# Kernel tuning notes

Measured on AMD Instinct MI355X. Metric: run time of the kernel, lower is better.

The kernel has to match this reference:

```python
import jax, jax.numpy as jnp
import numpy as np

DEPTH = 17                 # levels of the complete binary tree
N = 2**DEPTH - 1           # 131071 nodes, BFS order: children of n are 2n+1, 2n+2
IN_DIM = 128
HID = 128
OUT = 128


def setup_inputs() -> dict:
    key = jax.random.key(0)
    ks = jax.random.split(key, 20)

    def lin_w(k, o, i):
        s = 1.0 / np.sqrt(i)
        return jax.random.uniform(k, (o, i), minval=-s, maxval=s, dtype=jnp.float32)

    def lin_b(k, o, i):
        s = 1.0 / np.sqrt(i)
        return jax.random.uniform(k, (o,), minval=-s, maxval=s, dtype=jnp.float32)

    inp = {"x": jax.random.normal(ks[0], (N, IN_DIM), dtype=jnp.float32)}
    # complete binary tree, parent -> child edges (row0=src/parent, row1=dst/child)
    child = np.arange(1, N)
    parent = (child - 1) // 2
    inp["edge_index"] = jnp.asarray(np.stack([parent, child]), dtype=jnp.int32)
    names = [("Wi", "bWi", IN_DIM), ("Ui", "bUi", HID),
             ("Wf", "bWf", IN_DIM), ("Uf", "bUf", HID),
             ("Wo", "bWo", IN_DIM), ("Uo", "bUo", HID),
             ("Wu", "bWu", IN_DIM), ("Uu", "bUu", HID)]
    ki = 1
    for wname, bname, idim in names:
        inp[wname] = lin_w(ks[ki], HID, idim)
        inp[bname] = lin_b(ks[ki + 1], HID, idim)
        ki += 2
    inp["Wp"] = lin_w(ks[17], OUT, HID)
    inp["bWp"] = lin_b(ks[18], OUT, HID)
    return inp


def reference(x, edge_index, Wi, bWi, Ui, bUi, Wf, bWf, Uf, bUf,
              Wo, bWo, Uo, bUo, Wu, bWu, Uu, bUu, Wp, bWp):
    # edge_index encodes the complete binary tree in BFS order (children of n
    # are 2n+1 and 2n+2), so the recursion batches exactly by tree level.
    # Precompute input-side gate projections for ALL nodes in 4 GEMMs
    # (equivalent to calling W_*(x[node]) per node in the torch recursion).
    xi = x @ Wi.T + bWi            # (N, H)
    xf = x @ Wf.T + bWf
    xo = x @ Wo.T + bWo
    xu = x @ Wu.T + bWu

    h_next = None  # hidden states of the level below (children)
    c_next = None
    for d in range(DEPTH - 1, -1, -1):   # bottom-up over tree levels
        s = 2**d - 1                     # first node index of level d
        cnt = 2**d                       # nodes at level d
        li, lf, lo, lu = xi[s:s + cnt], xf[s:s + cnt], xo[s:s + cnt], xu[s:s + cnt]
        if h_next is None:               # leaves: no children, h_sum = 0
            i = jax.nn.sigmoid(li)
            o = jax.nn.sigmoid(lo)
            u = jnp.tanh(lu)
            c = i * u
        else:
            # children of node s+k are at positions 2(s+k)+1, 2(s+k)+2: contiguous
            ch_h = h_next.reshape(cnt, 2, HID)
            ch_c = c_next.reshape(cnt, 2, HID)
            h_sum = ch_h.sum(axis=1)     # child-sum
            i = jax.nn.sigmoid(li + h_sum @ Ui.T + bUi)
            o = jax.nn.sigmoid(lo + h_sum @ Uo.T + bUo)
            u = jnp.tanh(lu + h_sum @ Uu.T + bUu)
            # per-child forget gates: sigmoid(W_f x + U_f h_k)
            f = jax.nn.sigmoid(lf[:, None, :] + jnp.einsum('nkh,gh->nkg', ch_h, Uf) + bUf)
            c = i * u + (f * ch_c).sum(axis=1)
        h = o * jnp.tanh(c)
        h_next, c_next = h, c

    h_root = h_next[0]                   # root node index 0
    # dropout is identity in eval mode
    return h_root @ Wp.T + bWp           # (OUT,)
```

## Files before the change

kernel.cpp:

```cpp
#include <hip/hip_runtime.h>
#include <hip/hip_bf16.h>


#define DEPTH 17
#define NTREE ((1 << DEPTH) - 1)
#define DIM 128
#define XSTR 136
#define HSTR 136
#define CSTR 132

typedef __attribute__((ext_vector_type(8))) short short8;
typedef __attribute__((ext_vector_type(4))) float float4v;

__device__ __forceinline__ float sigm(float v) {
    return __fdividef(1.0f, 1.0f + __expf(-v));
}
__device__ __forceinline__ float ftanh(float v) {
    v = fminf(15.0f, fmaxf(-15.0f, v));
    float e = __expf(2.0f * v);
    return __fdividef(e - 1.0f, e + 1.0f);
}

__device__ __forceinline__ unsigned short f2bf(float f) {
    union { float f; unsigned u; } a; a.f = f;
    unsigned u = a.u;
    return (unsigned short)((u + 0x7fffu + ((u >> 16) & 1u)) >> 16);
}
__device__ __forceinline__ float bf2f(unsigned short s) {
    union { unsigned u; float f; } a; a.u = ((unsigned)s) << 16;
    return a.f;
}

struct WPtrs {
    const float* W[4];  const float* U[4];
    const float* bW[4]; const float* bU[4];
};

__global__ __launch_bounds__(256) void prep_kernel(WPtrs p, unsigned short* __restrict__ Bsw,
                                                   float* __restrict__ biasWU, float* __restrict__ biasL) {
    int idx = blockIdx.x * 256 + threadIdx.x;
    int j = idx & 7;
    int lane = (idx >> 3) & 63;
    int g = (idx >> 9) & 3;
    int ks = (idx >> 11) & 7;
    int w = idx >> 14;
    int L = lane & 15, q = lane >> 4;
    int c = w * 16 + L;
    int k = ks * 32 + q * 8 + j;
    float v = (k < 128) ? p.W[g][c * 128 + k] * (g == 3 ? 1.0f : 0.5f)
                        : p.U[g][c * 128 + (k - 128)];
    Bsw[idx] = f2bf(v);
    if (idx < 512) {
        int gg = idx >> 7, cc = idx & 127;
        biasWU[idx] = p.bW[gg][cc] + p.bU[gg][cc];
        biasL[idx]  = p.bW[gg][cc];
    }
}

__global__ __launch_bounds__(256) void convx_kernel(const float* __restrict__ x,
                                                    unsigned short* __restrict__ xbf, int n4) {
    int i = blockIdx.x * 256 + threadIdx.x;
    int stride = gridDim.x * 256;
    for (; i < n4; i += stride) {
        float4 v = ((const float4*)x)[i];
        ushort4 o;
        o.x = f2bf(v.x); o.y = f2bf(v.y); o.z = f2bf(v.z); o.w = f2bf(v.w);
        ((ushort4*)xbf)[i] = o;
    }
}

template <bool LEAF0>
__global__ __launch_bounds__(512, 2) void kd2_kernel(
    const unsigned short* __restrict__ xbf, const unsigned short* __restrict__ Bsw,
    const float* __restrict__ biasL, const float* __restrict__ biasWU,
    unsigned short* __restrict__ hbf, float* __restrict__ cbuf,
    int x0base, int x1base) {
    __shared__ __align__(16) unsigned short xs[48 * XSTR];
    __shared__ __align__(16) unsigned short hc[LEAF0 ? 16 : 64 * XSTR];
    __shared__ __align__(16) unsigned short h0[32 * XSTR];
    __shared__ __align__(16) unsigned short c0[32 * XSTR];
    __shared__ __align__(16) unsigned short hA1[16 * XSTR];
    __shared__ __align__(16) float cA1[16 * CSTR];

    const int tid = threadIdx.x;
    const int w = tid >> 6, lane = tid & 63, L = lane & 15, q = lane >> 4;
    const int ch = w * 16 + L;

    short8 b[32];
#pragma unroll
    for (int t = 0; t < 32; ++t)
        b[t] = *(const short8*)(Bsw + ((size_t)w << 14) + (t << 9) + lane * 8);

    const long n0 = (long)x0base + (long)blockIdx.x * 32;
    const long n1 = (long)x1base + (long)blockIdx.x * 16;
    const long cb = 2 * n0 + 1;

    for (int i = tid; i < 48 * 16; i += 512) {
        const int row = i >> 4, g = i & 15;
        const long node = (row < 32) ? (n0 + row) : (n1 + (row - 32));
        *(uint4*)(xs + row * XSTR + g * 8) = *(const uint4*)(xbf + (size_t)node * DIM + g * 8);
    }
    if (!LEAF0) {
        for (int i = tid; i < 64 * 16; i += 512) {
            const int row = i >> 4, g = i & 15;
            *(uint4*)(hc + row * XSTR + g * 8) = *(const uint4*)(hbf + (size_t)(cb + row) * DIM + g * 8);
        }
    }
    __syncthreads();

    if (LEAF0) {
        float4v acc[2][3];
#pragma unroll
        for (int mm = 0; mm < 2; ++mm)
#pragma unroll
            for (int g = 0; g < 3; ++g) acc[mm][g] = (float4v){0.f, 0.f, 0.f, 0.f};
#pragma unroll
        for (int ks = 0; ks < 4; ++ks) {
            short8 a[2];
            a[0] = *(const short8*)(xs + L * XSTR + ks * 32 + q * 8);
            a[1] = *(const short8*)(xs + (16 + L) * XSTR + ks * 32 + q * 8);
#pragma unroll
            for (int g = 0; g < 3; ++g)
#pragma unroll
                for (int mm = 0; mm < 2; ++mm)
                    acc[mm][g] = __builtin_amdgcn_mfma_f32_16x16x32_bf16(a[mm], b[ks * 4 + g], acc[mm][g], 0, 0, 0);
        }
#pragma unroll
        for (int mm = 0; mm < 2; ++mm)
#pragma unroll
            for (int r = 0; r < 4; ++r) {
                const int nl = 16 * mm + q * 4 + r;
                float iv = sigm(2.f * acc[mm][0][r] + biasL[ch]);
                float ov = sigm(2.f * acc[mm][1][r] + biasL[128 + ch]);
                float uv = ftanh(2.f * acc[mm][2][r] + biasL[256 + ch]);
                float cv = iv * uv;
                c0[nl * XSTR + ch] = f2bf(cv);
                h0[nl * XSTR + ch] = f2bf(ov * ftanh(cv));
            }
    } else {
        for (int mc = 0; mc < 4; mc += 2) {
            float4v acc[2][4];
#pragma unroll
            for (int mm = 0; mm < 2; ++mm)
#pragma unroll
                for (int g = 0; g < 4; ++g) acc[mm][g] = (float4v){0.f, 0.f, 0.f, 0.f};
#pragma unroll
            for (int ks = 0; ks < 8; ++ks) {
                const int kk = ks * 32;
                short8 a[2];
#pragma unroll
                for (int mm = 0; mm < 2; ++mm) {
                    if (kk < 128)
                        a[mm] = *(const short8*)(xs + (8 * (mc + mm) + (L >> 1)) * XSTR + kk + q * 8);
                    else
                        a[mm] = *(const short8*)(hc + (16 * (mc + mm) + L) * XSTR + (kk - 128) + q * 8);
                }
#pragma unroll
                for (int g = 0; g < 4; ++g)
#pragma unroll
                    for (int mm = 0; mm < 2; ++mm)
                        acc[mm][g] = __builtin_amdgcn_mfma_f32_16x16x32_bf16(a[mm], b[ks * 4 + g], acc[mm][g], 0, 0, 0);
            }
#pragma unroll
            for (int mm = 0; mm < 2; ++mm)
#pragma unroll
                for (int e = 0; e < 2; ++e) {
                    const int nl = 8 * (mc + mm) + 2 * q + e;
                    const int r0 = 2 * e, r1 = 2 * e + 1;
                    float iv = sigm(acc[mm][0][r0] + acc[mm][0][r1] + biasWU[ch]);
                    float ov = sigm(acc[mm][1][r0] + acc[mm][1][r1] + biasWU[128 + ch]);
                    float uv = ftanh(acc[mm][2][r0] + acc[mm][2][r1] + biasWU[256 + ch]);
                    float fl = sigm(acc[mm][3][r0] + biasWU[384 + ch]);
                    float fr = sigm(acc[mm][3][r1] + biasWU[384 + ch]);
                    float cl = cbuf[(size_t)(cb + 2 * nl) * DIM + ch];
                    float cr = cbuf[(size_t)(cb + 2 * nl + 1) * DIM + ch];
                    float cv = iv * uv + fl * cl + fr * cr;
                    c0[nl * XSTR + ch] = f2bf(cv);
                    h0[nl * XSTR + ch] = f2bf(ov * ftanh(cv));
                }
        }
    }
    __syncthreads();

    {
        float4v acc[2][4];
#pragma unroll
        for (int mm = 0; mm < 2; ++mm)
#pragma unroll
            for (int g = 0; g < 4; ++g) acc[mm][g] = (float4v){0.f, 0.f, 0.f, 0.f};
#pragma unroll
        for (int ks = 0; ks < 8; ++ks) {
            const int kk = ks * 32;
            short8 a[2];
#pragma unroll
            for (int mm = 0; mm < 2; ++mm) {
                if (kk < 128)
                    a[mm] = *(const short8*)(xs + (32 + 8 * mm + (L >> 1)) * XSTR + kk + q * 8);
                else
                    a[mm] = *(const short8*)(h0 + (16 * mm + L) * XSTR + (kk - 128) + q * 8);
            }
#pragma unroll
            for (int g = 0; g < 4; ++g)
#pragma unroll
                for (int mm = 0; mm < 2; ++mm)
                    acc[mm][g] = __builtin_amdgcn_mfma_f32_16x16x32_bf16(a[mm], b[ks * 4 + g], acc[mm][g], 0, 0, 0);
        }
#pragma unroll
        for (int mm = 0; mm < 2; ++mm)
#pragma unroll
            for (int e = 0; e < 2; ++e) {
                const int nl = 8 * mm + 2 * q + e;
                const int r0 = 2 * e, r1 = 2 * e + 1;
                float iv = sigm(acc[mm][0][r0] + acc[mm][0][r1] + biasWU[ch]);
                float ov = sigm(acc[mm][1][r0] + acc[mm][1][r1] + biasWU[128 + ch]);
                float uv = ftanh(acc[mm][2][r0] + acc[mm][2][r1] + biasWU[256 + ch]);
                float fl = sigm(acc[mm][3][r0] + biasWU[384 + ch]);
                float fr = sigm(acc[mm][3][r1] + biasWU[384 + ch]);
                float cl = bf2f(c0[(2 * nl) * XSTR + ch]);
                float cr = bf2f(c0[(2 * nl + 1) * XSTR + ch]);
                float cv = iv * uv + fl * cl + fr * cr;
                cA1[nl * CSTR + ch] = cv;
                hA1[nl * XSTR + ch] = f2bf(ov * ftanh(cv));
            }
    }
    __syncthreads();

    for (int i = tid; i < 16 * 16; i += 512) {
        const int row = i >> 4, g = i & 15;
        *(uint4*)(hbf + (size_t)(n1 + row) * DIM + g * 8) = *(const uint4*)(hA1 + row * XSTR + g * 8);
    }
    for (int i = tid; i < 16 * 32; i += 512) {
        const int row = i >> 5, j = i & 31;
        *(float4*)(cbuf + (size_t)(n1 + row) * DIM + j * 4) = *(const float4*)(cA1 + row * CSTR + j * 4);
    }
}

template <bool GCH>
__device__ __forceinline__ void internal_level(
    const unsigned short* xc,
    const unsigned short* hin_l, const float* cin_l,
    const unsigned short* __restrict__ hin_g, const float* __restrict__ cin_g, long cb,
    unsigned short* ho, int ho_str, float* co, int co_str, int cnt,
    const short8 (&b)[32], const float* __restrict__ biasWU,
    int L, int q, int ch) {
    const int rows = 2 * cnt;
    const int mt = (rows + 15) >> 4;
    for (int mc = 0; mc < mt; mc += 2) {
        const int mm_n = (mt - mc >= 2) ? 2 : 1;
        float4v acc[2][4];
#pragma unroll
        for (int mm = 0; mm < 2; ++mm)
#pragma unroll
            for (int g = 0; g < 4; ++g) acc[mm][g] = (float4v){0.f, 0.f, 0.f, 0.f};
#pragma unroll
        for (int ks = 0; ks < 8; ++ks) {
            const int kk = ks * 32;
            short8 a[2];
#pragma unroll
            for (int mm = 0; mm < 2; ++mm) {
                if (mm < mm_n) {
                    if (kk < 128) {
                        int xr = 8 * (mc + mm) + (L >> 1);
                        if (xr >= cnt) xr = 0;
                        a[mm] = *(const short8*)(xc + xr * XSTR + kk + q * 8);
                    } else if (!GCH) {
                        a[mm] = *(const short8*)(hin_l + (16 * (mc + mm) + L) * HSTR + (kk - 128) + q * 8);
                    } else {
                        a[mm] = *(const short8*)(hin_g + (size_t)(cb + 16 * (mc + mm) + L) * DIM + (kk - 128) + q * 8);
                    }
                }
            }
#pragma unroll
            for (int g = 0; g < 4; ++g)
#pragma unroll
                for (int mm = 0; mm < 2; ++mm)
                    if (mm < mm_n)
                        acc[mm][g] = __builtin_amdgcn_mfma_f32_16x16x32_bf16(a[mm], b[ks * 4 + g], acc[mm][g], 0, 0, 0);
        }
#pragma unroll
        for (int mm = 0; mm < 2; ++mm)
#pragma unroll
            for (int e = 0; e < 2; ++e) {
                if (mm < mm_n) {
                    const int nl = 8 * (mc + mm) + 2 * q + e;
                    if (nl < cnt) {
                        const int r0 = 2 * e, r1 = 2 * e + 1;
                        float iv = sigm(acc[mm][0][r0] + acc[mm][0][r1] + biasWU[ch]);
                        float ov = sigm(acc[mm][1][r0] + acc[mm][1][r1] + biasWU[128 + ch]);
                        float uv = ftanh(acc[mm][2][r0] + acc[mm][2][r1] + biasWU[256 + ch]);
                        float fl = sigm(acc[mm][3][r0] + biasWU[384 + ch]);
                        float fr = sigm(acc[mm][3][r1] + biasWU[384 + ch]);
                        float cl, cr;
                        if (!GCH) {
                            cl = cin_l[(2 * nl) * CSTR + ch];
                            cr = cin_l[(2 * nl + 1) * CSTR + ch];
                        } else {
                            cl = cin_g[(size_t)(cb + 2 * nl) * DIM + ch];
                            cr = cin_g[(size_t)(cb + 2 * nl + 1) * DIM + ch];
                        }
                        float cv = iv * uv + fl * cl + fr * cr;
                        co[nl * co_str + ch] = cv;
                        ho[nl * ho_str + ch] = f2bf(ov * ftanh(cv));
                    }
                }
            }
    }
}

template <int C, int NL, bool PROJ>
__global__ __launch_bounds__(512, 2) void k23_kernel(
    const unsigned short* __restrict__ xbf, const unsigned short* __restrict__ Bsw,
    const float* __restrict__ biasWU, unsigned short* __restrict__ hbf,
    float* __restrict__ cbuf, int d0,
    const float* __restrict__ Wp, const float* __restrict__ bWp,
    float* __restrict__ out) {
    constexpr int TOTX = 2 * C - (C >> (NL - 1));
    constexpr int AR = (C < 16) ? 16 : C;
    __shared__ __align__(16) unsigned short xs[TOTX * XSTR];
    __shared__ __align__(16) unsigned short hA[AR * HSTR];
    __shared__ __align__(16) unsigned short hB[16 * HSTR];
    __shared__ __align__(16) float cA[AR * CSTR];
    __shared__ __align__(16) float cB[16 * CSTR];
    __shared__ float red[4][128];

    const int tid = threadIdx.x;
    const int w = tid >> 6, lane = tid & 63, L = lane & 15, q = lane >> 4;
    const int ch = w * 16 + L;

    short8 b[32];
#pragma unroll
    for (int t = 0; t < 32; ++t)
        b[t] = *(const short8*)(Bsw + ((size_t)w << 14) + (t << 9) + lane * 8);

    {
        int xoff = 0;
#pragma unroll
        for (int l = 0; l < NL; ++l) {
            const int rows = C >> l;
            const long base = ((1 << (d0 - l)) - 1) + (long)blockIdx.x * rows;
            for (int i = tid; i < rows * 16; i += 512) {
                const int row = i >> 4, g = i & 15;
                *(uint4*)(xs + (xoff + row) * XSTR + g * 8) =
                    *(const uint4*)(xbf + (size_t)(base + row) * DIM + g * 8);
            }
            xoff += rows;
        }
    }
    __syncthreads();

    const long cb = ((1 << (d0 + 1)) - 1) + (long)blockIdx.x * (2 * C);
    internal_level<true>(xs, nullptr, nullptr, hbf, cbuf, cb,
                         hA, HSTR, cA, CSTR, C, b, biasWU, L, q, ch);
    __syncthreads();

    const unsigned short* hin = hA;
    const float* cin = cA;
    int xoff = C;
#pragma unroll
    for (int l = 1; l < NL; ++l) {
        const int cnt = C >> l;
        if (!PROJ && l == NL - 1) {
            const long ob = ((1 << (d0 - (NL - 1))) - 1) + (long)blockIdx.x;
            internal_level<false>(xs + xoff * XSTR, hin, cin, nullptr, nullptr, 0,
                                  hbf + (size_t)ob * DIM, DIM,
                                  cbuf + (size_t)ob * DIM, DIM, cnt, b, biasWU, L, q, ch);
        } else {
            unsigned short* ho = (l & 1) ? hB : hA;
            float* co = (l & 1) ? cB : cA;
            internal_level<false>(xs + xoff * XSTR, hin, cin, nullptr, nullptr, 0,
                                  ho, HSTR, co, CSTR, cnt, b, biasWU, L, q, ch);
            __syncthreads();
            hin = ho; cin = co;
        }
        xoff += cnt;
    }

    if (PROJ) {
        const int o = tid & 127, sg = tid >> 7;
        float pacc = 0.f;
#pragma unroll
        for (int jj = 0; jj < 8; ++jj) {
            const int k = sg * 32 + jj * 4;
            float4 wv = *(const float4*)(Wp + o * DIM + k);
            pacc += bf2f(hin[k]) * wv.x + bf2f(hin[k + 1]) * wv.y +
                    bf2f(hin[k + 2]) * wv.z + bf2f(hin[k + 3]) * wv.w;
        }
        red[sg][o] = pacc;
        __syncthreads();
        if (tid < 128) out[tid] = bWp[tid] + red[0][tid] + red[1][tid] + red[2][tid] + red[3][tid];
    }
}

extern "C" void kernel_launch(void* const* d_in, const int* in_sizes, int n_in,
                              void* d_out, int out_size, void* d_ws, size_t ws_size,
                              hipStream_t stream) {
    const float* x   = (const float*)d_in[0];
    const float* Wi  = (const float*)d_in[2];  const float* bWi = (const float*)d_in[3];
    const float* Ui  = (const float*)d_in[4];  const float* bUi = (const float*)d_in[5];
    const float* Wf  = (const float*)d_in[6];  const float* bWf = (const float*)d_in[7];
    const float* Uf  = (const float*)d_in[8];  const float* bUf = (const float*)d_in[9];
    const float* Wo  = (const float*)d_in[10]; const float* bWo = (const float*)d_in[11];
    const float* Uo  = (const float*)d_in[12]; const float* bUo = (const float*)d_in[13];
    const float* Wu  = (const float*)d_in[14]; const float* bWu = (const float*)d_in[15];
    const float* Uu  = (const float*)d_in[16]; const float* bUu = (const float*)d_in[17];
    const float* Wp  = (const float*)d_in[18]; const float* bWp = (const float*)d_in[19];

    unsigned short* Bsw = (unsigned short*)d_ws;
    float* biasWU = (float*)(Bsw + 131072);
    float* biasL  = biasWU + 512;
    float* cbuf   = biasL + 512;
    unsigned short* hbf = (unsigned short*)(cbuf + (size_t)65536 * DIM);
    unsigned short* xbf = hbf + (size_t)65536 * DIM;

    WPtrs p;
    p.W[0] = Wi; p.W[1] = Wo; p.W[2] = Wu; p.W[3] = Wf;
    p.U[0] = Ui; p.U[1] = Uo; p.U[2] = Uu; p.U[3] = Uf;
    p.bW[0] = bWi; p.bW[1] = bWo; p.bW[2] = bWu; p.bW[3] = bWf;
    p.bU[0] = bUi; p.bU[1] = bUo; p.bU[2] = bUu; p.bU[3] = bUf;

    prep_kernel<<<512, 256, 0, stream>>>(p, Bsw, biasWU, biasL);
    convx_kernel<<<4096, 256, 0, stream>>>(x, xbf, NTREE * 32);

    kd2_kernel<true><<<2048, 512, 0, stream>>>(xbf, Bsw, biasL, biasWU, hbf, cbuf,
                                               (1 << 16) - 1, (1 << 15) - 1);
    kd2_kernel<false><<<512, 512, 0, stream>>>(xbf, Bsw, biasL, biasWU, hbf, cbuf,
                                               (1 << 14) - 1, (1 << 13) - 1);
    kd2_kernel<false><<<128, 512, 0, stream>>>(xbf, Bsw, biasL, biasWU, hbf, cbuf,
                                               (1 << 12) - 1, (1 << 11) - 1);
    k23_kernel<32, 6, false><<<32, 512, 0, stream>>>(xbf, Bsw, biasWU, hbf, cbuf, 10,
                                                     nullptr, nullptr, nullptr);
    k23_kernel<16, 5, true><<<1, 512, 0, stream>>>(xbf, Bsw, biasWU, hbf, cbuf, 4,
                                                   Wp, bWp, (float*)d_out);
}
```

Before: 274.2 us.

## Fuse x bf16 conversion into level kernels and make them persistent with prefetch

```diff
diff --git a/kernel.cpp b/kernel.cpp
--- a/kernel.cpp
+++ b/kernel.cpp
@@ -57,24 +57,12 @@
     }
 }
 
-__global__ __launch_bounds__(256) void convx_kernel(const float* __restrict__ x,
-                                                    unsigned short* __restrict__ xbf, int n4) {
-    int i = blockIdx.x * 256 + threadIdx.x;
-    int stride = gridDim.x * 256;
-    for (; i < n4; i += stride) {
-        float4 v = ((const float4*)x)[i];
-        ushort4 o;
-        o.x = f2bf(v.x); o.y = f2bf(v.y); o.z = f2bf(v.z); o.w = f2bf(v.w);
-        ((ushort4*)xbf)[i] = o;
-    }
-}
-
 template <bool LEAF0>
-__global__ __launch_bounds__(512, 2) void kd2_kernel(
-    const unsigned short* __restrict__ xbf, const unsigned short* __restrict__ Bsw,
+__global__ __launch_bounds__(512, 2) void kd2p_kernel(
+    const float* __restrict__ x, const unsigned short* __restrict__ Bsw,
     const float* __restrict__ biasL, const float* __restrict__ biasWU,
     unsigned short* __restrict__ hbf, float* __restrict__ cbuf,
-    int x0base, int x1base) {
+    int x0base, int x1base, int ntiles) {
     __shared__ __align__(16) unsigned short xs[48 * XSTR];
     __shared__ __align__(16) unsigned short hc[LEAF0 ? 16 : 64 * XSTR];
     __shared__ __align__(16) unsigned short h0[32 * XSTR];
@@ -91,54 +79,130 @@
     for (int t = 0; t < 32; ++t)
         b[t] = *(const short8*)(Bsw + ((size_t)w << 14) + (t << 9) + lane * 8);
 
-    const long n0 = (long)x0base + (long)blockIdx.x * 32;
-    const long n1 = (long)x1base + (long)blockIdx.x * 16;
-    const long cb = 2 * n0 + 1;
-
-    for (int i = tid; i < 48 * 16; i += 512) {
-        const int row = i >> 4, g = i & 15;
-        const long node = (row < 32) ? (n0 + row) : (n1 + (row - 32));
-        *(uint4*)(xs + row * XSTR + g * 8) = *(const uint4*)(xbf + (size_t)node * DIM + g * 8);
-    }
-    if (!LEAF0) {
-        for (int i = tid; i < 64 * 16; i += 512) {
-            const int row = i >> 4, g = i & 15;
-            *(uint4*)(hc + row * XSTR + g * 8) = *(const uint4*)(hbf + (size_t)(cb + row) * DIM + g * 8);
-        }
-    }
-    __syncthreads();
-
-    if (LEAF0) {
-        float4v acc[2][3];
-#pragma unroll
-        for (int mm = 0; mm < 2; ++mm)
-#pragma unroll
-            for (int g = 0; g < 3; ++g) acc[mm][g] = (float4v){0.f, 0.f, 0.f, 0.f};
-#pragma unroll
-        for (int ks = 0; ks < 4; ++ks) {
-            short8 a[2];
-            a[0] = *(const short8*)(xs + L * XSTR + ks * 32 + q * 8);
-            a[1] = *(const short8*)(xs + (16 + L) * XSTR + ks * 32 + q * 8);
-#pragma unroll
-            for (int g = 0; g < 3; ++g)
+    float4 pfx[3];
+    {
+        const long tt = blockIdx.x;
+        const long n0 = (long)x0base + tt * 32, n1 = (long)x1base + tt * 16;
+#pragma unroll
+        for (int k = 0; k < 3; ++k) {
+            const int i = tid + 512 * k;
+            const int row = i >> 5, j = i & 31;
+            const long node = (row < 32) ? (n0 + row) : (n1 + (row - 32));
+            pfx[k] = *(const float4*)(x + (size_t)node * DIM + j * 4);
+        }
+    }
+
+    for (int it = 0; it < ntiles; ++it) {
+        const long tt = (long)it * gridDim.x + blockIdx.x;
+        const long n0 = (long)x0base + tt * 32;
+        const long n1 = (long)x1base + tt * 16;
+        const long cb = 2 * n0 + 1;
+
+#pragma unroll
+        for (int k = 0; k < 3; ++k) {
+            const int i = tid + 512 * k;
+            const int row = i >> 5, j = i & 31;
+            ushort4 o;
+            o.x = f2bf(pfx[k].x); o.y = f2bf(pfx[k].y);
+            o.z = f2bf(pfx[k].z); o.w = f2bf(pfx[k].w);
+            *(ushort4*)(xs + row * XSTR + j * 4) = o;
+        }
+        if (!LEAF0) {
+            for (int i = tid; i < 64 * 16; i += 512) {
+                const int row = i >> 4, g = i & 15;
+                *(uint4*)(hc + row * XSTR + g * 8) =
+                    *(const uint4*)(hbf + (size_t)(cb + row) * DIM + g * 8);
+            }
+        }
+        __syncthreads();
+
+        if (it + 1 < ntiles) {
+            const long tn = tt + gridDim.x;
+            const long m0 = (long)x0base + tn * 32, m1 = (long)x1base + tn * 16;
+#pragma unroll
+            for (int k = 0; k < 3; ++k) {
+                const int i = tid + 512 * k;
+                const int row = i >> 5, j = i & 31;
+                const long node = (row < 32) ? (m0 + row) : (m1 + (row - 32));
+                pfx[k] = *(const float4*)(x + (size_t)node * DIM + j * 4);
+            }
+        }
+
+        if (LEAF0) {
+            float4v acc[2][3];
+#pragma unroll
+            for (int mm = 0; mm < 2; ++mm)
+#pragma unroll
+                for (int g = 0; g < 3; ++g) acc[mm][g] = (float4v){0.f, 0.f, 0.f, 0.f};
+#pragma unroll
+            for (int ks = 0; ks < 4; ++ks) {
+                short8 a[2];
+                a[0] = *(const short8*)(xs + L * XSTR + ks * 32 + q * 8);
+                a[1] = *(const short8*)(xs + (16 + L) * XSTR + ks * 32 + q * 8);
+#pragma unroll
+                for (int g = 0; g < 3; ++g)
+#pragma unroll
+                    for (int mm = 0; mm < 2; ++mm)
+                        acc[mm][g] = __builtin_amdgcn_mfma_f32_16x16x32_bf16(a[mm], b[ks * 4 + g], acc[mm][g], 0, 0, 0);
+            }
+#pragma unroll
+            for (int mm = 0; mm < 2; ++mm)
+#pragma unroll
+                for (int r = 0; r < 4; ++r) {
+                    const int nl = 16 * mm + q * 4 + r;
+                    float iv = sigm(2.f * acc[mm][0][r] + biasL[ch]);
+                    float ov = sigm(2.f * acc[mm][1][r] + biasL[128 + ch]);
+                    float uv = ftanh(2.f * acc[mm][2][r] + biasL[256 + ch]);
+                    float cv = iv * uv;
+                    c0[nl * XSTR + ch] = f2bf(cv);
+                    h0[nl * XSTR + ch] = f2bf(ov * ftanh(cv));
+                }
+        } else {
+            for (int mc = 0; mc < 4; mc += 2) {
+                float4v acc[2][4];
 #pragma unroll
                 for (int mm = 0; mm < 2; ++mm)
-                    acc[mm][g] = __builtin_amdgcn_mfma_f32_16x16x32_bf16(a[mm], b[ks * 4 + g], acc[mm][g], 0, 0, 0);
-        }
-#pragma unroll
-        for (int mm = 0; mm < 2; ++mm)
-#pragma unroll
-            for (int r = 0; r < 4; ++r) {
-                const int nl = 16 * mm + q * 4 + r;
-                float iv = sigm(2.f * acc[mm][0][r] + biasL[ch]);
-                float ov = sigm(2.f * acc[mm][1][r] + biasL[128 + ch]);
-                float uv = ftanh(2.f * acc[mm][2][r] + biasL[256 + ch]);
-                float cv = iv * uv;
-                c0[nl * XSTR + ch] = f2bf(cv);
-                h0[nl * XSTR + ch] = f2bf(ov * ftanh(cv));
-            }
-    } else {
-        for (int mc = 0; mc < 4; mc += 2) {
+#pragma unroll
+                    for (int g = 0; g < 4; ++g) acc[mm][g] = (float4v){0.f, 0.f, 0.f, 0.f};
+#pragma unroll
+                for (int ks = 0; ks < 8; ++ks) {
+                    const int kk = ks * 32;
+                    short8 a[2];
+#pragma unroll
+                    for (int mm = 0; mm < 2; ++mm) {
+                        if (kk < 128)
+                            a[mm] = *(const short8*)(xs + (8 * (mc + mm) + (L >> 1)) * XSTR + kk + q * 8);
+                        else
+                            a[mm] = *(const short8*)(hc + (16 * (mc + mm) + L) * XSTR + (kk - 128) + q * 8);
+                    }
+#pragma unroll
+                    for (int g = 0; g < 4; ++g)
+#pragma unroll
+                        for (int mm = 0; mm < 2; ++mm)
+                            acc[mm][g] = __builtin_amdgcn_mfma_f32_16x16x32_bf16(a[mm], b[ks * 4 + g], acc[mm][g], 0, 0, 0);
+                }
+#pragma unroll
+                for (int mm = 0; mm < 2; ++mm)
+#pragma unroll
+                    for (int e = 0; e < 2; ++e) {
+                        const int nl = 8 * (mc + mm) + 2 * q + e;
+                        const int r0 = 2 * e, r1 = 2 * e + 1;
+                        float iv = sigm(acc[mm][0][r0] + acc[mm][0][r1] + biasWU[ch]);
+                        float ov = sigm(acc[mm][1][r0] + acc[mm][1][r1] + biasWU[128 + ch]);
+                        float uv = ftanh(acc[mm][2][r0] + acc[mm][2][r1] + biasWU[256 + ch]);
+                        float fl = sigm(acc[mm][3][r0] + biasWU[384 + ch]);
+                        float fr = sigm(acc[mm][3][r1] + biasWU[384 + ch]);
+                        float cl = cbuf[(size_t)(cb + 2 * nl) * DIM + ch];
+                        float cr = cbuf[(size_t)(cb + 2 * nl + 1) * DIM + ch];
+                        float cv = iv * uv + fl * cl + fr * cr;
+                        c0[nl * XSTR + ch] = f2bf(cv);
+                        h0[nl * XSTR + ch] = f2bf(ov * ftanh(cv));
+                    }
+            }
+        }
+        __syncthreads();
+
+        {
             float4v acc[2][4];
 #pragma unroll
             for (int mm = 0; mm < 2; ++mm)
@@ -151,9 +215,9 @@
 #pragma unroll
                 for (int mm = 0; mm < 2; ++mm) {
                     if (kk < 128)
-                        a[mm] = *(const short8*)(xs + (8 * (mc + mm) + (L >> 1)) * XSTR + kk + q * 8);
+                        a[mm] = *(const short8*)(xs + (32 + 8 * mm + (L >> 1)) * XSTR + kk + q * 8);
                     else
-                        a[mm] = *(const short8*)(hc + (16 * (mc + mm) + L) * XSTR + (kk - 128) + q * 8);
+                        a[mm] = *(const short8*)(h0 + (16 * mm + L) * XSTR + (kk - 128) + q * 8);
                 }
 #pragma unroll
                 for (int g = 0; g < 4; ++g)
@@ -165,73 +229,30 @@
             for (int mm = 0; mm < 2; ++mm)
 #pragma unroll
                 for (int e = 0; e < 2; ++e) {
-                    const int nl = 8 * (mc + mm) + 2 * q + e;
+                    const int nl = 8 * mm + 2 * q + e;
                     const int r0 = 2 * e, r1 = 2 * e + 1;
                     float iv = sigm(acc[mm][0][r0] + acc[mm][0][r1] + biasWU[ch]);
                     float ov = sigm(acc[mm][1][r0] + acc[mm][1][r1] + biasWU[128 + ch]);
                     float uv = ftanh(acc[mm][2][r0] + acc[mm][2][r1] + biasWU[256 + ch]);
                     float fl = sigm(acc[mm][3][r0] + biasWU[384 + ch]);
                     float fr = sigm(acc[mm][3][r1] + biasWU[384 + ch]);
-                    float cl = cbuf[(size_t)(cb + 2 * nl) * DIM + ch];
-                    float cr = cbuf[(size_t)(cb + 2 * nl + 1) * DIM + ch];
+                    float cl = bf2f(c0[(2 * nl) * XSTR + ch]);
+                    float cr = bf2f(c0[(2 * nl + 1) * XSTR + ch]);
                     float cv = iv * uv + fl * cl + fr * cr;
-                    c0[nl * XSTR + ch] = f2bf(cv);
-                    h0[nl * XSTR + ch] = f2bf(ov * ftanh(cv));
-                }
-        }
-    }
-    __syncthreads();
-
-    {
-        float4v acc[2][4];
-#pragma unroll
-        for (int mm = 0; mm < 2; ++mm)
-#pragma unroll
-            for (int g = 0; g < 4; ++g) acc[mm][g] = (float4v){0.f, 0.f, 0.f, 0.f};
-#pragma unroll
-        for (int ks = 0; ks < 8; ++ks) {
-            const int kk = ks * 32;
-            short8 a[2];
-#pragma unroll
-            for (int mm = 0; mm < 2; ++mm) {
-                if (kk < 128)
-                    a[mm] = *(const short8*)(xs + (32 + 8 * mm + (L >> 1)) * XSTR + kk + q * 8);
-                else
-                    a[mm] = *(const short8*)(h0 + (16 * mm + L) * XSTR + (kk - 128) + q * 8);
-            }
-#pragma unroll
-            for (int g = 0; g < 4; ++g)
-#pragma unroll
-                for (int mm = 0; mm < 2; ++mm)
-                    acc[mm][g] = __builtin_amdgcn_mfma_f32_16x16x32_bf16(a[mm], b[ks * 4 + g], acc[mm][g], 0, 0, 0);
-        }
-#pragma unroll
-        for (int mm = 0; mm < 2; ++mm)
-#pragma unroll
-            for (int e = 0; e < 2; ++e) {
-                const int nl = 8 * mm + 2 * q + e;
-                const int r0 = 2 * e, r1 = 2 * e + 1;
-                float iv = sigm(acc[mm][0][r0] + acc[mm][0][r1] + biasWU[ch]);
-                float ov = sigm(acc[mm][1][r0] + acc[mm][1][r1] + biasWU[128 + ch]);
-                float uv = ftanh(acc[mm][2][r0] + acc[mm][2][r1] + biasWU[256 + ch]);
-                float fl = sigm(acc[mm][3][r0] + biasWU[384 + ch]);
-                float fr = sigm(acc[mm][3][r1] + biasWU[384 + ch]);
-                float cl = bf2f(c0[(2 * nl) * XSTR + ch]);
-                float cr = bf2f(c0[(2 * nl + 1) * XSTR + ch]);
-                float cv = iv * uv + fl * cl + fr * cr;
-                cA1[nl * CSTR + ch] = cv;
-                hA1[nl * XSTR + ch] = f2bf(ov * ftanh(cv));
-            }
-    }
-    __syncthreads();
-
-    for (int i = tid; i < 16 * 16; i += 512) {
-        const int row = i >> 4, g = i & 15;
-        *(uint4*)(hbf + (size_t)(n1 + row) * DIM + g * 8) = *(const uint4*)(hA1 + row * XSTR + g * 8);
-    }
-    for (int i = tid; i < 16 * 32; i += 512) {
-        const int row = i >> 5, j = i & 31;
-        *(float4*)(cbuf + (size_t)(n1 + row) * DIM + j * 4) = *(const float4*)(cA1 + row * CSTR + j * 4);
+                    cA1[nl * CSTR + ch] = cv;
+                    hA1[nl * XSTR + ch] = f2bf(ov * ftanh(cv));
+                }
+        }
+        __syncthreads();
+
+        for (int i = tid; i < 16 * 16; i += 512) {
+            const int row = i >> 4, g = i & 15;
+            *(uint4*)(hbf + (size_t)(n1 + row) * DIM + g * 8) = *(const uint4*)(hA1 + row * XSTR + g * 8);
+        }
+        for (int i = tid; i < 16 * 32; i += 512) {
+            const int row = i >> 5, j = i & 31;
+            *(float4*)(cbuf + (size_t)(n1 + row) * DIM + j * 4) = *(const float4*)(cA1 + row * CSTR + j * 4);
+        }
     }
 }
 
@@ -309,7 +330,7 @@
 
 template <int C, int NL, bool PROJ>
 __global__ __launch_bounds__(512, 2) void k23_kernel(
-    const unsigned short* __restrict__ xbf, const unsigned short* __restrict__ Bsw,
+    const float* __restrict__ x, const unsigned short* __restrict__ Bsw,
     const float* __restrict__ biasWU, unsigned short* __restrict__ hbf,
     float* __restrict__ cbuf, int d0,
     const float* __restrict__ Wp, const float* __restrict__ bWp,
@@ -338,10 +359,12 @@
         for (int l = 0; l < NL; ++l) {
             const int rows = C >> l;
             const long base = ((1 << (d0 - l)) - 1) + (long)blockIdx.x * rows;
-            for (int i = tid; i < rows * 16; i += 512) {
-                const int row = i >> 4, g = i & 15;
-                *(uint4*)(xs + (xoff + row) * XSTR + g * 8) =
-                    *(const uint4*)(xbf + (size_t)(base + row) * DIM + g * 8);
+            for (int i = tid; i < rows * 32; i += 512) {
+                const int row = i >> 5, j = i & 31;
+                float4 v = *(const float4*)(x + (size_t)(base + row) * DIM + j * 4);
+                ushort4 o;
+                o.x = f2bf(v.x); o.y = f2bf(v.y); o.z = f2bf(v.z); o.w = f2bf(v.w);
+                *(ushort4*)(xs + (xoff + row) * XSTR + j * 4) = o;
             }
             xoff += rows;
         }
@@ -410,7 +433,6 @@
     float* biasL  = biasWU + 512;
     float* cbuf   = biasL + 512;
     unsigned short* hbf = (unsigned short*)(cbuf + (size_t)65536 * DIM);
-    unsigned short* xbf = hbf + (size_t)65536 * DIM;
 
     WPtrs p;
     p.W[0] = Wi; p.W[1] = Wo; p.W[2] = Wu; p.W[3] = Wf;
@@ -419,16 +441,15 @@
     p.bU[0] = bUi; p.bU[1] = bUo; p.bU[2] = bUu; p.bU[3] = bUf;
 
     prep_kernel<<<512, 256, 0, stream>>>(p, Bsw, biasWU, biasL);
-    convx_kernel<<<4096, 256, 0, stream>>>(x, xbf, NTREE * 32);
-
-    kd2_kernel<true><<<2048, 512, 0, stream>>>(xbf, Bsw, biasL, biasWU, hbf, cbuf,
-                                               (1 << 16) - 1, (1 << 15) - 1);
-    kd2_kernel<false><<<512, 512, 0, stream>>>(xbf, Bsw, biasL, biasWU, hbf, cbuf,
-                                               (1 << 14) - 1, (1 << 13) - 1);
-    kd2_kernel<false><<<128, 512, 0, stream>>>(xbf, Bsw, biasL, biasWU, hbf, cbuf,
-                                               (1 << 12) - 1, (1 << 11) - 1);
-    k23_kernel<32, 6, false><<<32, 512, 0, stream>>>(xbf, Bsw, biasWU, hbf, cbuf, 10,
+
+    kd2p_kernel<true><<<256, 512, 0, stream>>>(x, Bsw, biasL, biasWU, hbf, cbuf,
+                                               (1 << 16) - 1, (1 << 15) - 1, 8);
+    kd2p_kernel<false><<<256, 512, 0, stream>>>(x, Bsw, biasL, biasWU, hbf, cbuf,
+                                                (1 << 14) - 1, (1 << 13) - 1, 2);
+    kd2p_kernel<false><<<128, 512, 0, stream>>>(x, Bsw, biasL, biasWU, hbf, cbuf,
+                                                (1 << 12) - 1, (1 << 11) - 1, 1);
+    k23_kernel<32, 6, false><<<32, 512, 0, stream>>>(x, Bsw, biasWU, hbf, cbuf, 10,
                                                      nullptr, nullptr, nullptr);
-    k23_kernel<16, 5, true><<<1, 512, 0, stream>>>(xbf, Bsw, biasWU, hbf, cbuf, 4,
+    k23_kernel<16, 5, true><<<1, 512, 0, stream>>>(x, Bsw, biasWU, hbf, cbuf, 4,
                                                    Wp, bWp, (float*)d_out);
 }
```

After: 244.0 us. 11.0% less time.
